# Optimization experiments

Hardware: AMD Instinct MI355X
Metric: run time of the kernel (lower is better)

Reference implementation:

```python
import jax, jax.numpy as jnp
import numpy as np

V = 32000   # src and trg vocab
E = 256     # embed dim
H = 512     # hidden dim
S, T, B = 50, 40, 32


def lstm_layer(x, h0, c0, Wih, Whh, b):
    # x: [T,B,Din]; PyTorch gate order i,f,g,o; b = b_ih + b_hh (identical math)
    def step(carry, xt):
        h, c = carry
        g = xt @ Wih.T + h @ Whh.T + b
        i, f, gg, o = jnp.split(g, 4, axis=-1)
        c = jax.nn.sigmoid(f) * c + jax.nn.sigmoid(i) * jnp.tanh(gg)
        h = jax.nn.sigmoid(o) * jnp.tanh(c)
        return (h, c), h
    (hT, cT), ys = jax.lax.scan(step, (h0, c0), x)
    return ys, hT, cT


def setup_inputs() -> dict:
    key = jax.random.key(0)
    ks = jax.random.split(key, 20)
    s = 0.05
    d = {
        'src': jax.random.randint(ks[0], (S, B), 0, V),
        'trg': jax.random.randint(ks[1], (T, B), 0, V),
        'enc_emb': jax.random.normal(ks[2], (V, E), jnp.float32) * s,
        'enc_Wih0': jax.random.normal(ks[3], (4 * H, E), jnp.float32) * s,
        'enc_Whh0': jax.random.normal(ks[4], (4 * H, H), jnp.float32) * s,
        'enc_b0': jax.random.normal(ks[5], (4 * H,), jnp.float32) * s,
        'enc_Wih1': jax.random.normal(ks[6], (4 * H, H), jnp.float32) * s,
        'enc_Whh1': jax.random.normal(ks[7], (4 * H, H), jnp.float32) * s,
        'enc_b1': jax.random.normal(ks[8], (4 * H,), jnp.float32) * s,
        'dec_emb': jax.random.normal(ks[9], (V, E), jnp.float32) * s,
        'dec_Wih0': jax.random.normal(ks[10], (4 * H, E), jnp.float32) * s,
        'dec_Whh0': jax.random.normal(ks[11], (4 * H, H), jnp.float32) * s,
        'dec_b0': jax.random.normal(ks[12], (4 * H,), jnp.float32) * s,
        'dec_Wih1': jax.random.normal(ks[13], (4 * H, H), jnp.float32) * s,
        'dec_Whh1': jax.random.normal(ks[14], (4 * H, H), jnp.float32) * s,
        'dec_b1': jax.random.normal(ks[15], (4 * H,), jnp.float32) * s,
        'out_W': jax.random.normal(ks[16], (V, H), jnp.float32) * s,
        'out_b': jax.random.normal(ks[17], (V,), jnp.float32) * s,
    }
    return d


def reference(src, trg, enc_emb, enc_Wih0, enc_Whh0, enc_b0, enc_Wih1, enc_Whh1, enc_b1,
              dec_emb, dec_Wih0, dec_Whh0, dec_b0, dec_Wih1, dec_Whh1, dec_b1, out_W, out_b):
    Bsz = src.shape[1]
    z = jnp.zeros((Bsz, H), enc_emb.dtype)
    # Encoder: 2-layer LSTM over src embeddings (dropout=0)
    x = enc_emb[src]                                    # [S,B,E]
    ys0, h0, c0 = lstm_layer(x, z, z, enc_Wih0, enc_Whh0, enc_b0)
    _, h1, c1 = lstm_layer(ys0, z, z, enc_Wih1, enc_Whh1, enc_b1)
    # Decoder with teacherForcingRatio=1.0: inputs are trg[:-1]
    dx = dec_emb[trg[:-1]]                              # [T-1,B,E]
    dy0, _, _ = lstm_layer(dx, h0, c0, dec_Wih0, dec_Whh0, dec_b0)
    dy1, _, _ = lstm_layer(dy0, h1, c1, dec_Wih1, dec_Whh1, dec_b1)
    logits = jnp.einsum('tbh,vh->tbv', dy1, out_W) + out_b  # [T-1,B,V]
    outputs = jnp.concatenate([jnp.zeros((1, Bsz, out_W.shape[0]), logits.dtype), logits], axis=0)
    return outputs
```

## Files before the change

kernel.cpp:

```cpp
#include <hip/hip_runtime.h>
#include <hip/hip_bf16.h>
#include <stdint.h>

typedef unsigned short ushort_t;

#define HID 512
#define FOURH 2048
#define BSZ 32
#define SLEN 50
#define TDEC 39
#define EMB 256
#define VOC 32000

using short8  = __attribute__((ext_vector_type(8))) short;
using float4v = __attribute__((ext_vector_type(4))) float;

__device__ inline float bf16lo(uint32_t u) { return __uint_as_float(u << 16); }
__device__ inline float bf16hi(uint32_t u) { return __uint_as_float(u & 0xffff0000u); }

__device__ inline ushort_t f32_to_bf16(float f) {
    uint32_t u = __float_as_uint(f);
    uint32_t r = (u + 0x7fffu + ((u >> 16) & 1u)) >> 16;
    return (ushort_t)r;
}

__device__ inline float sigmoid_f(float x) { return 1.0f / (1.0f + expf(-x)); }

__device__ inline int detect_f32(const ushort_t* __restrict__ probe) {
    int cnt = 0;
#pragma unroll
    for (int i = 0; i < 64; ++i) {
        int e = (probe[i] >> 7) & 0xFF;
        cnt += (e >= 0x8A);
    }
    return cnt > 0;
}

__global__ void embed_kernel(const int* __restrict__ idx,
                             const void* __restrict__ emb,
                             uint32_t* __restrict__ out,
                             int total_u,
                             const ushort_t* __restrict__ probe)
{
    const int F32 = detect_f32(probe);
    int i = blockIdx.x * 256 + threadIdx.x;
    if (i >= total_u) return;
    int tok = i >> 7;
    int col = i & 127;
    int row = idx[tok];
    if (F32) {
        const float* ef = (const float*)emb + (size_t)row * EMB + col * 2;
        uint32_t lo = f32_to_bf16(ef[0]);
        uint32_t hi = f32_to_bf16(ef[1]);
        out[i] = lo | (hi << 16);
    } else {
        out[i] = ((const uint32_t*)emb)[(size_t)row * 128 + col];
    }
}

__device__ inline float load_bias(const void* __restrict__ bias, int n, int F32) {
    if (F32) return ((const float*)bias)[n];
    return __uint_as_float(((uint32_t)((const ushort_t*)bias)[n]) << 16);
}

__device__ inline void gload_lds16(const ushort_t* __restrict__ g, ushort_t* l) {
    __builtin_amdgcn_global_load_lds(
        (const __attribute__((address_space(1))) uint32_t*)g,
        (__attribute__((address_space(3))) uint32_t*)l,
        16, 0, 0);
}

template <int SMODE>
__global__ __launch_bounds__(256, 2)
void gemm_tile_kernel(const ushort_t* __restrict__ A,
                      const void* __restrict__ W,
                      const void* __restrict__ bias,
                      void* __restrict__ C,
                      int M, int N, int K,
                      const ushort_t* __restrict__ probe)
{
    const int F32 = detect_f32(probe);
    __shared__ ushort_t Alds[128 * 64];
    __shared__ ushort_t Blds[128 * 64];

    const int tid  = threadIdx.x;
    const int lane = tid & 63;
    const int wave = tid >> 6;
    const int l16  = lane & 15;
    const int l4   = lane >> 4;

    const int wm = (wave >> 1) * 64;
    const int wn = (wave & 1) * 64;

    const int mbase = blockIdx.x * 128;
    const int nbase = blockIdx.y * 128;

    const int sr   = lane >> 3;
    const int scol = ((lane & 7) ^ sr) * 8;

    float4v acc[4][4];
#pragma unroll
    for (int i = 0; i < 4; ++i)
#pragma unroll
        for (int j = 0; j < 4; ++j) acc[i][j] = (float4v){0.f, 0.f, 0.f, 0.f};

    for (int k0 = 0; k0 < K; k0 += 64) {
        __syncthreads();

#pragma unroll
        for (int c = 0; c < 4; ++c) {
            int chunk = wave * 4 + c;
            int row   = chunk * 8 + sr;
            gload_lds16(A + (size_t)(mbase + row) * K + k0 + scol,
                        Alds + chunk * 512);
        }
        if (F32) {
#pragma unroll
            for (int c = 0; c < 4; ++c) {
                int chunk = wave * 4 + c;
                int row   = chunk * 8 + sr;
                const float* gp = (const float*)W + (size_t)(nbase + row) * K + k0 + scol;
                float4v f0 = *(const float4v*)gp;
                float4v f1 = *(const float4v*)(gp + 4);
                short8 v;
#pragma unroll
                for (int j = 0; j < 4; ++j) v[j]     = (short)f32_to_bf16(f0[j]);
#pragma unroll
                for (int j = 0; j < 4; ++j) v[4 + j] = (short)f32_to_bf16(f1[j]);
                *(short8*)(Blds + chunk * 512 + lane * 8) = v;
            }
        } else {
#pragma unroll
            for (int c = 0; c < 4; ++c) {
                int chunk = wave * 4 + c;
                int row   = chunk * 8 + sr;
                gload_lds16((const ushort_t*)W + (size_t)(nbase + row) * K + k0 + scol,
                            Blds + chunk * 512);
            }
        }
        __syncthreads();

        short8 af[4][2], bf[4][2];
#pragma unroll
        for (int mi = 0; mi < 4; ++mi) {
            int row = wm + mi * 16 + l16;
#pragma unroll
            for (int kk = 0; kk < 2; ++kk) {
                int cb = (kk * 64 + l4 * 16) ^ ((l16 & 7) << 4);
                af[mi][kk] = *(const short8*)((const char*)Alds + row * 128 + cb);
            }
        }
#pragma unroll
        for (int ni = 0; ni < 4; ++ni) {
            int row = wn + ni * 16 + l16;
#pragma unroll
            for (int kk = 0; kk < 2; ++kk) {
                int cb = (kk * 64 + l4 * 16) ^ ((l16 & 7) << 4);
                bf[ni][kk] = *(const short8*)((const char*)Blds + row * 128 + cb);
            }
        }
#pragma unroll
        for (int mi = 0; mi < 4; ++mi)
#pragma unroll
            for (int ni = 0; ni < 4; ++ni) {
                acc[mi][ni] = __builtin_amdgcn_mfma_f32_16x16x32_bf16(
                    af[mi][0], bf[ni][0], acc[mi][ni], 0, 0, 0);
                acc[mi][ni] = __builtin_amdgcn_mfma_f32_16x16x32_bf16(
                    af[mi][1], bf[ni][1], acc[mi][ni], 0, 0, 0);
            }
    }

#pragma unroll
    for (int mi = 0; mi < 4; ++mi) {
#pragma unroll
        for (int ni = 0; ni < 4; ++ni) {
            int n = nbase + wn + ni * 16 + l16;
            float bv = load_bias(bias, n, F32);
#pragma unroll
            for (int r = 0; r < 4; ++r) {
                int m = mbase + wm + mi * 16 + l4 * 4 + r;
                if (m < M) {
                    float v = acc[mi][ni][r] + bv;
                    if (SMODE == 0) {
                        ((float*)C)[(size_t)m * N + n] = v;
                    } else {
                        size_t idx = (size_t)(BSZ + m) * N + n;
                        if (F32) ((float*)C)[idx] = v;
                        else     ((ushort_t*)C)[idx] = f32_to_bf16(v);
                    }
                }
            }
        }
    }
}

__global__ void lstm_step_kernel(const float* __restrict__ xih,
                                 const ushort_t* __restrict__ h_in,
                                 ushort_t* __restrict__ h_out,
                                 float* __restrict__ c,
                                 const void* __restrict__ Whh,
                                 ushort_t* __restrict__ ys,
                                 const ushort_t* __restrict__ probe)
{
    const int F32 = detect_f32(probe);
    __shared__ uint32_t h_lds[BSZ * 257];
    __shared__ uint32_t w_lds[8 * 256];
    __shared__ float    g_lds[8][BSZ];

    const int tid = threadIdx.x;
    const int j0  = blockIdx.x * 2;

    const uint32_t* h32 = (const uint32_t*)h_in;
#pragma unroll
    for (int i = 0; i < 32; ++i) {
        int idx = tid + i * 256;
        int row = idx >> 8, col = idx & 255;
        h_lds[row * 257 + col] = h32[idx];
    }

#pragma unroll
    for (int i = 0; i < 8; ++i) {
        int idx  = tid + i * 256;
        int lrr  = idx >> 8, col = idx & 255;
        int gate = lrr >> 1, jl = lrr & 1;
        size_t wrow = (size_t)(gate * HID + j0 + jl);
        if (F32) {
            const float* wf = (const float*)Whh + wrow * HID + col * 2;
            uint32_t lo = f32_to_bf16(wf[0]);
            uint32_t hi = f32_to_bf16(wf[1]);
            w_lds[lrr * 256 + col] = lo | (hi << 16);
        } else {
            w_lds[lrr * 256 + col] = ((const uint32_t*)Whh)[wrow * 256 + col];
        }
    }
    __syncthreads();

    const int b    = tid & 31;
    const int lr   = tid >> 5;
    const int gate = lr >> 1;
    const int jl   = lr & 1;

    float dot = xih[b * FOURH + gate * HID + j0 + jl];
    const uint32_t* hr = &h_lds[b * 257];
    const uint32_t* wr = &w_lds[lr * 256];
    float s0 = 0.f, s1 = 0.f;
#pragma unroll 8
    for (int k = 0; k < 256; ++k) {
        uint32_t hu = hr[k], wu = wr[k];
        s0 += bf16lo(hu) * bf16lo(wu);
        s1 += bf16hi(hu) * bf16hi(wu);
    }
    g_lds[lr][b] = dot + s0 + s1;
    __syncthreads();

    if (tid < 64) {
        int b2 = tid & 31, jl2 = tid >> 5;
        int j  = j0 + jl2;
        float gi = g_lds[(0 << 1) | jl2][b2];
        float gf = g_lds[(1 << 1) | jl2][b2];
        float gg = g_lds[(2 << 1) | jl2][b2];
        float go = g_lds[(3 << 1) | jl2][b2];
        float cold = c[b2 * HID + j];
        float cn = sigmoid_f(gf) * cold + sigmoid_f(gi) * tanhf(gg);
        float hn = sigmoid_f(go) * tanhf(cn);
        c[b2 * HID + j] = cn;
        ushort_t hb = f32_to_bf16(hn);
        h_out[b2 * HID + j] = hb;
        if (ys) ys[b2 * HID + j] = hb;
    }
}

__global__ void zero_row_kernel(void* __restrict__ outv,
                                const ushort_t* __restrict__ probe)
{
    const int F32 = detect_f32(probe);
    int i = blockIdx.x * 256 + threadIdx.x;
    if (i >= BSZ * VOC) return;
    if (F32) ((uint32_t*)outv)[i] = 0u;
    else     ((ushort_t*)outv)[i] = 0;
}

extern "C" void kernel_launch(void* const* d_in, const int* in_sizes, int n_in,
                              void* d_out, int out_size, void* d_ws, size_t ws_size,
                              hipStream_t stream)
{
    const int*      src      = (const int*)d_in[0];
    const int*      trg      = (const int*)d_in[1];
    const void*     enc_emb  = d_in[2];
    const void*     enc_Wih0 = d_in[3];
    const void*     enc_Whh0 = d_in[4];
    const void*     enc_b0   = d_in[5];
    const void*     enc_Wih1 = d_in[6];
    const void*     enc_Whh1 = d_in[7];
    const void*     enc_b1   = d_in[8];
    const void*     dec_emb  = d_in[9];
    const void*     dec_Wih0 = d_in[10];
    const void*     dec_Whh0 = d_in[11];
    const void*     dec_b0   = d_in[12];
    const void*     dec_Wih1 = d_in[13];
    const void*     dec_Whh1 = d_in[14];
    const void*     dec_b1   = d_in[15];
    const void*     out_W    = d_in[16];
    const void*     out_b    = d_in[17];

    const ushort_t* probe = (const ushort_t*)enc_b0;

    const int ME = SLEN * BSZ;
    const int MD = TDEC * BSZ;

    ushort_t* dy1 = (ushort_t*)d_out;

    char*  arena = (char*)d_out + (4u << 20);
    size_t aoff  = 0;
    auto acarve = [&](size_t bytes) -> void* {
        void* p = arena + aoff;
        aoff = (aoff + bytes + 255) & ~(size_t)255;
        return p;
    };
    const size_t HSTATE = (size_t)BSZ * HID;
    float*    Xbig = (float*)acarve((size_t)ME * FOURH * 4);
    ushort_t* X0   = (ushort_t*)acarve((size_t)ME * EMB * 2);
    ushort_t* DX0  = (ushort_t*)acarve((size_t)MD * EMB * 2);
    ushort_t* ys0  = (ushort_t*)acarve((size_t)ME * HID * 2);
    ushort_t* dy0  = (ushort_t*)acarve((size_t)MD * HID * 2);
    ushort_t* h0b  = (ushort_t*)acarve(2 * HSTATE * 2);
    float*    c0b  = (float*)acarve(HSTATE * 4);
    ushort_t* h1b  = (ushort_t*)acarve(2 * HSTATE * 2);
    float*    c1b  = (float*)acarve(HSTATE * 4);

    hipMemsetAsync(h0b, 0, HSTATE * 2, stream);
    hipMemsetAsync(c0b, 0, HSTATE * 4, stream);
    hipMemsetAsync(h1b, 0, HSTATE * 2, stream);
    hipMemsetAsync(c1b, 0, HSTATE * 4, stream);

    {
        int tu = ME * (EMB / 2);
        embed_kernel<<<(tu + 255) / 256, 256, 0, stream>>>(
            src, enc_emb, (uint32_t*)X0, tu, probe);
        int td = MD * (EMB / 2);
        embed_kernel<<<(td + 255) / 256, 256, 0, stream>>>(
            trg, dec_emb, (uint32_t*)DX0, td, probe);
    }

    const size_t XIH_T = (size_t)BSZ * FOURH;
    const int MTE = (ME + 127) / 128;
    const int MTD = (MD + 127) / 128;

    gemm_tile_kernel<0><<<dim3(MTE, FOURH / 128), 256, 0, stream>>>(
        X0, enc_Wih0, enc_b0, Xbig, ME, FOURH, EMB, probe);
    for (int t = 0; t < SLEN; ++t) {
        lstm_step_kernel<<<256, 256, 0, stream>>>(
            Xbig + (size_t)t * XIH_T,
            h0b + (t & 1) * HSTATE, h0b + ((t + 1) & 1) * HSTATE,
            c0b, enc_Whh0, ys0 + (size_t)t * HSTATE, probe);
    }
    gemm_tile_kernel<0><<<dim3(MTE, FOURH / 128), 256, 0, stream>>>(
        ys0, enc_Wih1, enc_b1, Xbig, ME, FOURH, HID, probe);
    for (int t = 0; t < SLEN; ++t) {
        lstm_step_kernel<<<256, 256, 0, stream>>>(
            Xbig + (size_t)t * XIH_T,
            h1b + (t & 1) * HSTATE, h1b + ((t + 1) & 1) * HSTATE,
            c1b, enc_Whh1, (ushort_t*)nullptr, probe);
    }

    gemm_tile_kernel<0><<<dim3(MTD, FOURH / 128), 256, 0, stream>>>(
        DX0, dec_Wih0, dec_b0, Xbig, MD, FOURH, EMB, probe);
    for (int t = 0; t < TDEC; ++t) {
        lstm_step_kernel<<<256, 256, 0, stream>>>(
            Xbig + (size_t)t * XIH_T,
            h0b + (t & 1) * HSTATE, h0b + ((t + 1) & 1) * HSTATE,
            c0b, dec_Whh0, dy0 + (size_t)t * HSTATE, probe);
    }
    gemm_tile_kernel<0><<<dim3(MTD, FOURH / 128), 256, 0, stream>>>(
        dy0, dec_Wih1, dec_b1, Xbig, MD, FOURH, HID, probe);
    for (int t = 0; t < TDEC; ++t) {
        lstm_step_kernel<<<256, 256, 0, stream>>>(
            Xbig + (size_t)t * XIH_T,
            h1b + (t & 1) * HSTATE, h1b + ((t + 1) & 1) * HSTATE,
            c1b, dec_Whh1, dy1 + (size_t)t * HSTATE, probe);
    }

    gemm_tile_kernel<1><<<dim3(MTD, VOC / 128), 256, 0, stream>>>(
        dy1, out_W, out_b, d_out, MD, VOC, HID, probe);

    zero_row_kernel<<<(BSZ * VOC + 255) / 256, 256, 0, stream>>>(d_out, probe);
}
```

Before: 2.194 ms.

## Run each LSTM layer as one persistent cooperative kernel with grid sync

Replaces 178 per-timestep LSTM step launches with four persistent cooperative kernels, one per layer. Each of 64 blocks keeps its slice of Whh in LDS for all timesteps, holds the cell state in registers, and computes the recurrent matmul with bf16 MFMA; timesteps are separated by grid.sync. This removes per-step launch overhead and repeated weight reloads, at the cost of using only 64 blocks and paying a grid-wide barrier each step. If the cooperative launch fails, it falls back to the old per-step kernels.

Result: slower. 4.239 ms (+93.2%).

```diff
diff --git a/kernel.cpp b/kernel.cpp
--- a/kernel.cpp
+++ b/kernel.cpp
@@ -1,6 +1,9 @@
 #include <hip/hip_runtime.h>
 #include <hip/hip_bf16.h>
+#include <hip/hip_cooperative_groups.h>
 #include <stdint.h>
+
+namespace cg = cooperative_groups;
 
 typedef unsigned short ushort_t;
 
@@ -194,6 +197,129 @@
     }
 }
 
+__global__ __launch_bounds__(256, 1)
+void lstm_layer_kernel(const float* __restrict__ xih,
+                       ushort_t* __restrict__ hbuf,
+                       float*    __restrict__ cbuf,
+                       const void* __restrict__ Whh,
+                       ushort_t* __restrict__ ys,
+                       const ushort_t* __restrict__ probe,
+                       int T)
+{
+    const int F32 = detect_f32(probe);
+    cg::grid_group grid = cg::this_grid();
+
+    __shared__ ushort_t w_lds[32 * 512];
+    __shared__ ushort_t h_lds[32 * 512];
+
+    const int tid  = threadIdx.x;
+    const int lane = tid & 63;
+    const int wave = tid >> 6;
+    const int l16  = lane & 15;
+    const int quad = lane >> 4;
+    const int j0   = blockIdx.x * 8;
+
+    const int m0 = (wave >> 1) * 16;
+    const int ni = wave & 1;
+
+#pragma unroll
+    for (int i = 0; i < 8; ++i) {
+        int idx = tid + i * 256;
+        int rr  = idx >> 6;
+        int c16 = idx & 63;
+        int gate = rr & 3, u8 = rr >> 2;
+        size_t grow = (size_t)(gate * HID + j0 + u8) * HID + c16 * 8;
+        short8 v;
+        if (F32) {
+            const float* gp = (const float*)Whh + grow;
+            float4v f0 = *(const float4v*)gp;
+            float4v f1 = *(const float4v*)(gp + 4);
+#pragma unroll
+            for (int j = 0; j < 4; ++j) v[j]     = (short)f32_to_bf16(f0[j]);
+#pragma unroll
+            for (int j = 0; j < 4; ++j) v[4 + j] = (short)f32_to_bf16(f1[j]);
+        } else {
+            v = *(const short8*)((const ushort_t*)Whh + grow);
+        }
+        *(short8*)((char*)w_lds + rr * 1024 + ((c16 * 16) ^ ((rr & 7) << 4))) = v;
+    }
+
+    const int u8me = ni * 4 + (l16 >> 2);
+    const int gme  = l16 & 3;
+    const int jme  = j0 + u8me;
+
+    float creg[4];
+#pragma unroll
+    for (int r = 0; r < 4; ++r)
+        creg[r] = cbuf[(m0 + quad * 4 + r) * HID + jme];
+
+    const bool has_ys = (ys != nullptr);
+
+    for (int t = 0; t < T; ++t) {
+        const ushort_t* hin  = hbuf + (size_t)(t & 1) * (BSZ * HID);
+        ushort_t*       hout = hbuf + (size_t)((t + 1) & 1) * (BSZ * HID);
+        const float*    xr   = xih + (size_t)t * (BSZ * FOURH);
+
+        float xv[4];
+#pragma unroll
+        for (int r = 0; r < 4; ++r)
+            xv[r] = xr[(m0 + quad * 4 + r) * FOURH + gme * HID + jme];
+
+#pragma unroll
+        for (int i = 0; i < 8; ++i) {
+            int idx = tid + i * 256;
+            int b   = idx >> 6;
+            int c16 = idx & 63;
+            short8 v = *(const short8*)(hin + (size_t)b * HID + c16 * 8);
+            *(short8*)((char*)h_lds + b * 1024 + ((c16 * 16) ^ ((b & 7) << 4))) = v;
+        }
+        __syncthreads();
+
+        float4v acc = (float4v){0.f, 0.f, 0.f, 0.f};
+#pragma unroll
+        for (int kk = 0; kk < 16; ++kk) {
+            int cb = (kk * 64 + quad * 16) ^ ((l16 & 7) << 4);
+            short8 a = *(const short8*)((const char*)h_lds + (m0 + l16) * 1024 + cb);
+            short8 b = *(const short8*)((const char*)w_lds + (ni * 16 + l16) * 1024 + cb);
+            acc = __builtin_amdgcn_mfma_f32_16x16x32_bf16(a, b, acc, 0, 0, 0);
+        }
+
+#pragma unroll
+        for (int r = 0; r < 4; ++r) {
+            float g   = acc[r] + xv[r];
+            float arg = (gme == 2) ? 2.f * g : g;
+            float s   = 1.f / (1.f + expf(-arg));
+            float act = (gme == 2) ? 2.f * s - 1.f : s;
+            int base = lane & ~3;
+            float ai = __shfl(act, base + 0);
+            float af = __shfl(act, base + 1);
+            float ag = __shfl(act, base + 2);
+            float ao = __shfl(act, base + 3);
+            if (gme == 0) {
+                float cn = af * creg[r] + ai * ag;
+                creg[r] = cn;
+                float th = 2.f / (1.f + expf(-2.f * cn)) - 1.f;
+                float hn = ao * th;
+                ushort_t hb = f32_to_bf16(hn);
+                int b = m0 + quad * 4 + r;
+                hout[b * HID + jme] = hb;
+                if (has_ys) ys[(size_t)t * (BSZ * HID) + b * HID + jme] = hb;
+            }
+        }
+
+        __syncthreads();
+        __threadfence();
+        grid.sync();
+        __threadfence();
+    }
+
+    if (gme == 0) {
+#pragma unroll
+        for (int r = 0; r < 4; ++r)
+            cbuf[(m0 + quad * 4 + r) * HID + jme] = creg[r];
+    }
+}
+
 __global__ void lstm_step_kernel(const float* __restrict__ xih,
                                  const ushort_t* __restrict__ h_in,
                                  ushort_t* __restrict__ h_out,
@@ -217,7 +343,6 @@
         int row = idx >> 8, col = idx & 255;
         h_lds[row * 257 + col] = h32[idx];
     }
-
 #pragma unroll
     for (int i = 0; i < 8; ++i) {
         int idx  = tid + i * 256;
@@ -346,39 +471,42 @@
     const int MTE = (ME + 127) / 128;
     const int MTD = (MD + 127) / 128;
 
+    auto launch_lstm = [&](const float* xih, ushort_t* hb, float* cb,
+                           const void* Whh, ushort_t* ysp, int T) {
+        const float* a0 = xih; ushort_t* a1 = hb; float* a2 = cb;
+        const void* a3 = Whh; ushort_t* a4 = ysp;
+        const ushort_t* a5 = probe; int a6 = T;
+        void* ka[] = {(void*)&a0, (void*)&a1, (void*)&a2, (void*)&a3,
+                      (void*)&a4, (void*)&a5, (void*)&a6};
+        hipError_t e = hipLaunchCooperativeKernel(
+            reinterpret_cast<const void*>(&lstm_layer_kernel),
+            dim3(64), dim3(256), ka, 0, stream);
+        if (e != hipSuccess) {
+            for (int t = 0; t < T; ++t)
+                lstm_step_kernel<<<256, 256, 0, stream>>>(
+                    xih + (size_t)t * XIH_T,
+                    hb + (t & 1) * HSTATE, hb + ((t + 1) & 1) * HSTATE,
+                    cb, Whh,
+                    ysp ? ysp + (size_t)t * HSTATE : (ushort_t*)nullptr,
+                    probe);
+        }
+    };
+
     gemm_tile_kernel<0><<<dim3(MTE, FOURH / 128), 256, 0, stream>>>(
         X0, enc_Wih0, enc_b0, Xbig, ME, FOURH, EMB, probe);
-    for (int t = 0; t < SLEN; ++t) {
-        lstm_step_kernel<<<256, 256, 0, stream>>>(
-            Xbig + (size_t)t * XIH_T,
-            h0b + (t & 1) * HSTATE, h0b + ((t + 1) & 1) * HSTATE,
-            c0b, enc_Whh0, ys0 + (size_t)t * HSTATE, probe);
-    }
+    launch_lstm(Xbig, h0b, c0b, enc_Whh0, ys0, SLEN);
+
     gemm_tile_kernel<0><<<dim3(MTE, FOURH / 128), 256, 0, stream>>>(
         ys0, enc_Wih1, enc_b1, Xbig, ME, FOURH, HID, probe);
-    for (int t = 0; t < SLEN; ++t) {
-        lstm_step_kernel<<<256, 256, 0, stream>>>(
-            Xbig + (size_t)t * XIH_T,
-            h1b + (t & 1) * HSTATE, h1b + ((t + 1) & 1) * HSTATE,
-            c1b, enc_Whh1, (ushort_t*)nullptr, probe);
-    }
+    launch_lstm(Xbig, h1b, c1b, enc_Whh1, (ushort_t*)nullptr, SLEN);
 
     gemm_tile_kernel<0><<<dim3(MTD, FOURH / 128), 256, 0, stream>>>(
         DX0, dec_Wih0, dec_b0, Xbig, MD, FOURH, EMB, probe);
-    for (int t = 0; t < TDEC; ++t) {
-        lstm_step_kernel<<<256, 256, 0, stream>>>(
-            Xbig + (size_t)t * XIH_T,
-            h0b + (t & 1) * HSTATE, h0b + ((t + 1) & 1) * HSTATE,
-            c0b, dec_Whh0, dy0 + (size_t)t * HSTATE, probe);
-    }
+    launch_lstm(Xbig, h0b, c0b, dec_Whh0, dy0, TDEC);
+
     gemm_tile_kernel<0><<<dim3(MTD, FOURH / 128), 256, 0, stream>>>(
         dy0, dec_Wih1, dec_b1, Xbig, MD, FOURH, HID, probe);
-    for (int t = 0; t < TDEC; ++t) {
-        lstm_step_kernel<<<256, 256, 0, stream>>>(
-            Xbig + (size_t)t * XIH_T,
-            h1b + (t & 1) * HSTATE, h1b + ((t + 1) & 1) * HSTATE,
-            c1b, dec_Whh1, dy1 + (size_t)t * HSTATE, probe);
-    }
+    launch_lstm(Xbig, h1b, c1b, dec_Whh1, dy1, TDEC);
 
     gemm_tile_kernel<1><<<dim3(MTD, VOC / 128), 256, 0, stream>>>(
         dy1, out_W, out_b, d_out, MD, VOC, HID, probe);
```
